# Kernel optimization log

Hardware: AMD Instinct MI355X
Metric: run time of the kernel (lower is better)

## Reference

```python
import jax, jax.numpy as jnp
import numpy as np

BETA = 2.0  # init kwarg beta


def _roi_map(roi_params, H, W):
    # roi_params: (N, K, 4) = (mu_x, mu_y, sigma_x, sigma_y) in [0, 1]
    dtype = roi_params.dtype
    gx = (jnp.arange(W, dtype=dtype) + 0.5) / W  # x-coords of grid columns
    gy = (jnp.arange(H, dtype=dtype) + 0.5) / H  # y-coords of grid rows
    mu_x, mu_y = roi_params[:, :, 0], roi_params[:, :, 1]
    sg_x, sg_y = roi_params[:, :, 2], roi_params[:, :, 3]
    # separable generalized-Gaussian log pdf along each axis
    log_x = -(jnp.abs(gx[None, None, :] - mu_x[:, :, None]) / sg_x[:, :, None]) ** BETA  # (N,K,W)
    log_y = -(jnp.abs(gy[None, None, :] - mu_y[:, :, None]) / sg_y[:, :, None]) ** BETA  # (N,K,H)
    scores = jnp.exp(log_y[:, :, :, None] + log_x[:, :, None, :])  # (N,K,H,W)
    mx = jnp.max(scores, axis=(2, 3), keepdims=True)
    return scores / (mx + 1e-12)  # max-normalized attention maps


def setup_inputs() -> dict:
    key = jax.random.key(0)
    k1, k2 = jax.random.split(key)
    x = jax.random.normal(k1, (16, 128, 128, 256), dtype=jnp.float32)
    roi_params = jax.random.uniform(k2, (16, 64, 4), dtype=jnp.float32)
    return {"x": x, "roi_params": roi_params}


def reference(x, roi_params):
    N, H, W, d = x.shape
    roi_map = _roi_map(roi_params, H, W)           # (N,K,H,W)
    flat_map = roi_map.reshape(N, -1, H * W)        # (N,K,HW)
    flat_feats = x.reshape(N, H * W, d)             # (N,HW,d)
    roi_features = jnp.einsum('nrf,nfd->nrd', flat_map, flat_feats) / (H * W)
    return roi_features, roi_params, roi_map
```

## Files before the change

### kernel.cpp

```cpp
#include <hip/hip_runtime.h>
#include <hip/hip_bf16.h>
#include <math.h>

#define NB 16
#define RB 64
#define HB 128
#define WB 128
#define DB 256
#define HW (HB * WB)

typedef __attribute__((ext_vector_type(8))) short bf16x8;
typedef __attribute__((ext_vector_type(4))) short short4v;
typedef __attribute__((ext_vector_type(4))) float f32x4;

static __device__ __forceinline__ short f2bf(float f) {
  __hip_bfloat16 h = __float2bfloat16(f);
  return *reinterpret_cast<short*>(&h);
}
static __device__ __forceinline__ float bf2f(short s) {
  return __uint_as_float(((unsigned)(unsigned short)s) << 16);
}

static __device__ __forceinline__ float axis_maxlog(float mu, float sg) {
  int i = (int)roundf(mu * 128.0f - 0.5f);
  i = i < 0 ? 0 : (i > 127 ? 127 : i);
  const float g = (i + 0.5f) * (1.0f / 128.0f);
  const float tm = fabsf(g - mu) / sg;
  return -(tm * tm);
}

__global__ __launch_bounds__(512, 4) void feat_kernel(
    const float* __restrict__ x, const float* __restrict__ roi,
    short* __restrict__ partials) {
  __shared__ float buf[2][32 * DB];

  const int bid = blockIdx.x;
  const int n   = bid >> 5;
  const int kc  = bid & 31;
  const int t   = threadIdx.x;
  const int l   = t & 63;
  const int wv  = t >> 6;
  const int mh  = wv >> 2;
  const int dw  = wv & 3;
  const int l15 = l & 15;
  const int lk  = (l >> 4) * 8;
  const int h0  = kc * 4;
  const int dbase = dw * 64 + l15 * 4;

  const f32x4* gx4 =
      reinterpret_cast<const f32x4*>(x + ((size_t)n * HW + (size_t)kc * 512) * DB);

  float mux[2], c2x[2], mlx[2];
  float eyv[4][2];
#pragma unroll
  for (int rf = 0; rf < 2; ++rf) {
    const int nr = n * RB + mh * 32 + rf * 16 + l15;
    const float4 rp = reinterpret_cast<const float4*>(roi)[nr];
    const float mlx_ = axis_maxlog(rp.x, rp.z);
    const float mly_ = axis_maxlog(rp.y, rp.w);
    const float em   = expf(mlx_ + mly_);
    const float s    = em / (em + 1e-12f);
    const float isx  = 1.0f / rp.z;
    mux[rf] = rp.x; c2x[rf] = isx * isx; mlx[rf] = mlx_;
#pragma unroll
    for (int hh = 0; hh < 4; ++hh) {
      const float g = (h0 + hh + 0.5f) * (1.0f / 128.0f);
      const float ty = fabsf(g - rp.y) / rp.w;
      eyv[hh][rf] = expf(-(ty * ty) - mly_) * s;
    }
  }

  f32x4 acc[2][4];
#pragma unroll
  for (int rf = 0; rf < 2; ++rf)
#pragma unroll
    for (int f = 0; f < 4; ++f) acc[rf][f] = (f32x4)0.0f;

  f32x4 g0, g1, g2, g3;
#define GLOAD(bi) do {                                                       \
    const f32x4* gp_ = gx4 + (size_t)(bi) * 2048;                            \
    g0 = gp_[t]; g1 = gp_[t + 512]; g2 = gp_[t + 1024]; g3 = gp_[t + 1536];  \
  } while (0)
#define DSWRITE(slot) do {                                                   \
    f32x4* lp_ = reinterpret_cast<f32x4*>(&buf[slot][0]);                    \
    lp_[t] = g0; lp_[t + 512] = g1; lp_[t + 1024] = g2; lp_[t + 1536] = g3;  \
  } while (0)

  GLOAD(0);
  DSWRITE(0);
  asm volatile("s_waitcnt lgkmcnt(0)" ::: "memory");
  __builtin_amdgcn_s_barrier();
  __builtin_amdgcn_sched_barrier(0);

#define KSTEP(bi) do {                                                       \
    if ((bi) < 15) GLOAD((bi) + 1);                                          \
    const float* bp_ = &buf[(bi) & 1][0];                                    \
    f32x4 xv_[8];                                                            \
    _Pragma("unroll")                                                        \
    for (int j = 0; j < 8; ++j)                                              \
      xv_[j] = *reinterpret_cast<const f32x4*>(                              \
          bp_ + (lk + j) * DB + dbase);                                      \
    bf16x8 bfr_[4];                                                          \
    _Pragma("unroll")                                                        \
    for (int f = 0; f < 4; ++f) {                                            \
      bf16x8 b_;                                                             \
      _Pragma("unroll")                                                      \
      for (int j = 0; j < 8; ++j) b_[j] = f2bf(xv_[j][f]);                   \
      bfr_[f] = b_;                                                          \
    }                                                                        \
    bf16x8 afr_[2];                                                          \
    _Pragma("unroll")                                                        \
    for (int rf = 0; rf < 2; ++rf) {                                         \
      const float ey_ = eyv[(bi) >> 2][rf];                                  \
      bf16x8 a_;                                                             \
      _Pragma("unroll")                                                      \
      for (int i = 0; i < 8; ++i) {                                          \
        const int col = ((bi) & 3) * 32 + lk + i;                            \
        const float g_ = (col + 0.5f) * (1.0f / 128.0f);                     \
        const float d_ = g_ - mux[rf];                                       \
        const float e_ = expf(-(d_ * d_ * c2x[rf]) - mlx[rf]);               \
        a_[i] = f2bf(ey_ * e_);                                              \
      }                                                                      \
      afr_[rf] = a_;                                                         \
    }                                                                        \
    _Pragma("unroll")                                                        \
    for (int rf = 0; rf < 2; ++rf)                                           \
      _Pragma("unroll")                                                      \
      for (int f = 0; f < 4; ++f)                                            \
        acc[rf][f] = __builtin_amdgcn_mfma_f32_16x16x32_bf16(                \
            afr_[rf], bfr_[f], acc[rf][f], 0, 0, 0);                         \
    if ((bi) < 15) DSWRITE(((bi) + 1) & 1);                                  \
    asm volatile("s_waitcnt lgkmcnt(0)" ::: "memory");                       \
    __builtin_amdgcn_s_barrier();                                            \
    __builtin_amdgcn_sched_barrier(0);                                       \
  } while (0)

  KSTEP(0);  KSTEP(1);  KSTEP(2);  KSTEP(3);
  KSTEP(4);  KSTEP(5);  KSTEP(6);  KSTEP(7);
  KSTEP(8);  KSTEP(9);  KSTEP(10); KSTEP(11);
  KSTEP(12); KSTEP(13); KSTEP(14); KSTEP(15);

#undef KSTEP
#undef DSWRITE
#undef GLOAD

  short* P = partials + (size_t)bid * (RB * DB);
#pragma unroll
  for (int rf = 0; rf < 2; ++rf) {
#pragma unroll
    for (int reg = 0; reg < 4; ++reg) {
      const int r = mh * 32 + rf * 16 + (l >> 4) * 4 + reg;
      short4v v;
      v.x = f2bf(acc[rf][0][reg]); v.y = f2bf(acc[rf][1][reg]);
      v.z = f2bf(acc[rf][2][reg]); v.w = f2bf(acc[rf][3][reg]);
      *reinterpret_cast<short4v*>(P + (size_t)r * DB + dbase) = v;
    }
  }
}

__global__ __launch_bounds__(512) void map_only_kernel(
    const float* __restrict__ roi, float* __restrict__ out_map) {
  __shared__ float sT[1024];
  const int mb = blockIdx.x;
  const int t  = threadIdx.x;
  float* sEx = sT;
  float* sEy = sT + 512;
  for (int v = t; v < 1024; v += 512) {
    const int rr = v >> 8, axis = (v >> 7) & 1, pos = v & 127;
    const float4 rp = reinterpret_cast<const float4*>(roi)[mb * 4 + rr];
    const float mlx = axis_maxlog(rp.x, rp.z);
    const float mly = axis_maxlog(rp.y, rp.w);
    const float em  = expf(mlx + mly);
    const float s   = em / (em + 1e-12f);
    const float g   = (pos + 0.5f) * (1.0f / 128.0f);
    if (axis == 0) {
      const float tx = fabsf(g - rp.x) / rp.z;
      sEx[rr * 128 + pos] = expf(-(tx * tx) - mlx);
    } else {
      const float ty = fabsf(g - rp.y) / rp.w;
      sEy[rr * 128 + pos] = expf(-(ty * ty) - mly) * s;
    }
  }
  __syncthreads();
  f32x4* dst = reinterpret_cast<f32x4*>(out_map + (size_t)mb * 4 * HW);
#pragma unroll
  for (int p = 0; p < 32; ++p) {
    const int idx = p * 512 + t;
    const int rr = idx >> 12, h = (idx >> 5) & 127, w4 = idx & 31;
    const f32x4 e = *reinterpret_cast<const f32x4*>(&sEx[rr * 128 + w4 * 4]);
    dst[idx] = e * (f32x4)sEy[rr * 128 + h];
  }
}

__global__ __launch_bounds__(256) void reduce_kernel(
    const short* __restrict__ partials, const float* __restrict__ roi,
    float* __restrict__ outF, float* __restrict__ out_params) {
  const int idx = blockIdx.x * 256 + threadIdx.x;
  const int n   = idx >> 12;
  const int i4  = idx & 4095;
  const short4v* p =
      reinterpret_cast<const short4v*>(partials) + (size_t)n * 32 * 4096 + i4;
  f32x4 s = (f32x4)0.0f;
#pragma unroll
  for (int kc = 0; kc < 32; ++kc) {
    const short4v v = p[(size_t)kc * 4096];
    s.x += bf2f(v.x); s.y += bf2f(v.y); s.z += bf2f(v.z); s.w += bf2f(v.w);
  }
  s *= (1.0f / (float)HW);
  reinterpret_cast<f32x4*>(outF)[idx] = s;
  if (idx < NB * RB * 4) out_params[idx] = roi[idx];
}

extern "C" void kernel_launch(void* const* d_in, const int* in_sizes, int n_in,
                              void* d_out, int out_size, void* d_ws, size_t ws_size,
                              hipStream_t stream) {
  const float* x   = (const float*)d_in[0];
  const float* roi = (const float*)d_in[1];
  float* out        = (float*)d_out;
  float* out_feat   = out;
  float* out_params = out + NB * RB * DB;
  float* out_map    = out_params + NB * RB * 4;

  const size_t par_shorts = 512u * RB * DB;
  const bool ws_ok = ws_size >= par_shorts * sizeof(short) + 64;

  short* P = ws_ok ? (short*)d_ws : (short*)out_map;

  feat_kernel<<<512, 512, 0, stream>>>(x, roi, P);
  reduce_kernel<<<256, 256, 0, stream>>>(P, roi, out_feat, out_params);
  map_only_kernel<<<256, 512, 0, stream>>>(roi, out_map);
}
```

Before: 99.62 us.

## Fuse map writer into feat kernel, drop LDS staging, widen per-wave ROI tile

```diff
diff --git a/kernel.cpp b/kernel.cpp
--- a/kernel.cpp
+++ b/kernel.cpp
@@ -8,6 +8,7 @@
 #define WB 128
 #define DB 256
 #define HW (HB * WB)
+#define LOG2E 1.4426950408889634f
 
 typedef __attribute__((ext_vector_type(8))) short bf16x8;
 typedef __attribute__((ext_vector_type(4))) short short4v;
@@ -29,39 +30,72 @@
   return -(tm * tm);
 }
 
-__global__ __launch_bounds__(512, 4) void feat_kernel(
+template <bool WITHMAP>
+__global__ __launch_bounds__(256, 2) void feat_kernel(
     const float* __restrict__ x, const float* __restrict__ roi,
-    short* __restrict__ partials) {
-  __shared__ float buf[2][32 * DB];
+    short* __restrict__ partials, float* __restrict__ out_map) {
+  __shared__ float sT[1024];
 
   const int bid = blockIdx.x;
+  const int t   = threadIdx.x;
+
+  if (WITHMAP && bid >= 512) {
+    const int mb = bid - 512;
+    float* sEx = sT;
+    float* sEy = sT + 512;
+    for (int v = t; v < 1024; v += 256) {
+      const int rr = v >> 8, axis = (v >> 7) & 1, pos = v & 127;
+      const float4 rp = reinterpret_cast<const float4*>(roi)[mb * 4 + rr];
+      const float mlx = axis_maxlog(rp.x, rp.z);
+      const float mly = axis_maxlog(rp.y, rp.w);
+      const float em  = expf(mlx + mly);
+      const float s   = em / (em + 1e-12f);
+      const float g   = (pos + 0.5f) * (1.0f / 128.0f);
+      if (axis == 0) {
+        const float tx = fabsf(g - rp.x) / rp.z;
+        sEx[rr * 128 + pos] = expf(-(tx * tx) - mlx);
+      } else {
+        const float ty = fabsf(g - rp.y) / rp.w;
+        sEy[rr * 128 + pos] = expf(-(ty * ty) - mly) * s;
+      }
+    }
+    __syncthreads();
+    f32x4* dst = reinterpret_cast<f32x4*>(out_map + (size_t)mb * 4 * HW);
+#pragma unroll 8
+    for (int p = 0; p < 64; ++p) {
+      const int idx = p * 256 + t;
+      const int rr = idx >> 12, h = (idx >> 5) & 127, w4 = idx & 31;
+      const f32x4 e = *reinterpret_cast<const f32x4*>(&sEx[rr * 128 + w4 * 4]);
+      dst[idx] = e * (f32x4)sEy[rr * 128 + h];
+    }
+    return;
+  }
+
   const int n   = bid >> 5;
-  const int kc  = bid & 31;
-  const int t   = threadIdx.x;
+  const int hc  = bid & 31;
   const int l   = t & 63;
   const int wv  = t >> 6;
-  const int mh  = wv >> 2;
-  const int dw  = wv & 3;
   const int l15 = l & 15;
   const int lk  = (l >> 4) * 8;
-  const int h0  = kc * 4;
-  const int dbase = dw * 64 + l15 * 4;
+  const int h0  = hc * 4;
+  const int dbase = wv * 64 + l15 * 4;
 
   const f32x4* gx4 =
-      reinterpret_cast<const f32x4*>(x + ((size_t)n * HW + (size_t)kc * 512) * DB);
-
-  float mux[2], c2x[2], mlx[2];
-  float eyv[4][2];
-#pragma unroll
-  for (int rf = 0; rf < 2; ++rf) {
-    const int nr = n * RB + mh * 32 + rf * 16 + l15;
+      reinterpret_cast<const f32x4*>(x + ((size_t)n * HW + (size_t)hc * 512) * DB);
+  const int lquad = wv * 16 + l15;
+
+  float mux[4], c2x[4], mlx2[4];
+  float eyv[4][4];
+#pragma unroll
+  for (int rf = 0; rf < 4; ++rf) {
+    const int nr = n * RB + rf * 16 + l15;
     const float4 rp = reinterpret_cast<const float4*>(roi)[nr];
     const float mlx_ = axis_maxlog(rp.x, rp.z);
     const float mly_ = axis_maxlog(rp.y, rp.w);
     const float em   = expf(mlx_ + mly_);
     const float s    = em / (em + 1e-12f);
     const float isx  = 1.0f / rp.z;
-    mux[rf] = rp.x; c2x[rf] = isx * isx; mlx[rf] = mlx_;
+    mux[rf] = rp.x; c2x[rf] = isx * isx * LOG2E; mlx2[rf] = mlx_ * LOG2E;
 #pragma unroll
     for (int hh = 0; hh < 4; ++hh) {
       const float g = (h0 + hh + 0.5f) * (1.0f / 128.0f);
@@ -70,47 +104,33 @@
     }
   }
 
-  f32x4 acc[2][4];
-#pragma unroll
-  for (int rf = 0; rf < 2; ++rf)
+  f32x4 acc[4][4];
+#pragma unroll
+  for (int rf = 0; rf < 4; ++rf)
 #pragma unroll
     for (int f = 0; f < 4; ++f) acc[rf][f] = (f32x4)0.0f;
 
-  f32x4 g0, g1, g2, g3;
-#define GLOAD(bi) do {                                                       \
-    const f32x4* gp_ = gx4 + (size_t)(bi) * 2048;                            \
-    g0 = gp_[t]; g1 = gp_[t + 512]; g2 = gp_[t + 1024]; g3 = gp_[t + 1536];  \
+  f32x4 xva[8], xvb[8];
+
+#define GLOAD(BUFN, bi) do {                                                 \
+    _Pragma("unroll")                                                        \
+    for (int j = 0; j < 8; ++j)                                              \
+      BUFN[j] = gx4[(size_t)((bi) * 32 + lk + j) * 64 + lquad];              \
   } while (0)
-#define DSWRITE(slot) do {                                                   \
-    f32x4* lp_ = reinterpret_cast<f32x4*>(&buf[slot][0]);                    \
-    lp_[t] = g0; lp_[t + 512] = g1; lp_[t + 1024] = g2; lp_[t + 1536] = g3;  \
-  } while (0)
-
-  GLOAD(0);
-  DSWRITE(0);
-  asm volatile("s_waitcnt lgkmcnt(0)" ::: "memory");
-  __builtin_amdgcn_s_barrier();
-  __builtin_amdgcn_sched_barrier(0);
-
-#define KSTEP(bi) do {                                                       \
-    if ((bi) < 15) GLOAD((bi) + 1);                                          \
-    const float* bp_ = &buf[(bi) & 1][0];                                    \
-    f32x4 xv_[8];                                                            \
-    _Pragma("unroll")                                                        \
-    for (int j = 0; j < 8; ++j)                                              \
-      xv_[j] = *reinterpret_cast<const f32x4*>(                              \
-          bp_ + (lk + j) * DB + dbase);                                      \
+
+#define KSTEP(bi, CUR, NXT) do {                                             \
+    if ((bi) < 15) GLOAD(NXT, (bi) + 1);                                     \
     bf16x8 bfr_[4];                                                          \
     _Pragma("unroll")                                                        \
     for (int f = 0; f < 4; ++f) {                                            \
       bf16x8 b_;                                                             \
       _Pragma("unroll")                                                      \
-      for (int j = 0; j < 8; ++j) b_[j] = f2bf(xv_[j][f]);                   \
+      for (int j = 0; j < 8; ++j) b_[j] = f2bf(CUR[j][f]);                   \
       bfr_[f] = b_;                                                          \
     }                                                                        \
-    bf16x8 afr_[2];                                                          \
-    _Pragma("unroll")                                                        \
-    for (int rf = 0; rf < 2; ++rf) {                                         \
+    bf16x8 afr_[4];                                                          \
+    _Pragma("unroll")                                                        \
+    for (int rf = 0; rf < 4; ++rf) {                                         \
       const float ey_ = eyv[(bi) >> 2][rf];                                  \
       bf16x8 a_;                                                             \
       _Pragma("unroll")                                                      \
@@ -118,38 +138,36 @@
         const int col = ((bi) & 3) * 32 + lk + i;                            \
         const float g_ = (col + 0.5f) * (1.0f / 128.0f);                     \
         const float d_ = g_ - mux[rf];                                       \
-        const float e_ = expf(-(d_ * d_ * c2x[rf]) - mlx[rf]);               \
+        const float e_ = exp2f(-(d_ * d_ * c2x[rf]) - mlx2[rf]);             \
         a_[i] = f2bf(ey_ * e_);                                              \
       }                                                                      \
       afr_[rf] = a_;                                                         \
     }                                                                        \
     _Pragma("unroll")                                                        \
-    for (int rf = 0; rf < 2; ++rf)                                           \
+    for (int rf = 0; rf < 4; ++rf)                                           \
       _Pragma("unroll")                                                      \
       for (int f = 0; f < 4; ++f)                                            \
         acc[rf][f] = __builtin_amdgcn_mfma_f32_16x16x32_bf16(                \
             afr_[rf], bfr_[f], acc[rf][f], 0, 0, 0);                         \
-    if ((bi) < 15) DSWRITE(((bi) + 1) & 1);                                  \
-    asm volatile("s_waitcnt lgkmcnt(0)" ::: "memory");                       \
-    __builtin_amdgcn_s_barrier();                                            \
-    __builtin_amdgcn_sched_barrier(0);                                       \
   } while (0)
 
-  KSTEP(0);  KSTEP(1);  KSTEP(2);  KSTEP(3);
-  KSTEP(4);  KSTEP(5);  KSTEP(6);  KSTEP(7);
-  KSTEP(8);  KSTEP(9);  KSTEP(10); KSTEP(11);
-  KSTEP(12); KSTEP(13); KSTEP(14); KSTEP(15);
+  GLOAD(xva, 0);
+  KSTEP(0,  xva, xvb); KSTEP(1,  xvb, xva); KSTEP(2,  xva, xvb);
+  KSTEP(3,  xvb, xva); KSTEP(4,  xva, xvb); KSTEP(5,  xvb, xva);
+  KSTEP(6,  xva, xvb); KSTEP(7,  xvb, xva); KSTEP(8,  xva, xvb);
+  KSTEP(9,  xvb, xva); KSTEP(10, xva, xvb); KSTEP(11, xvb, xva);
+  KSTEP(12, xva, xvb); KSTEP(13, xvb, xva); KSTEP(14, xva, xvb);
+  KSTEP(15, xvb, xva);
 
 #undef KSTEP
-#undef DSWRITE
 #undef GLOAD
 
   short* P = partials + (size_t)bid * (RB * DB);
 #pragma unroll
-  for (int rf = 0; rf < 2; ++rf) {
+  for (int rf = 0; rf < 4; ++rf) {
 #pragma unroll
     for (int reg = 0; reg < 4; ++reg) {
-      const int r = mh * 32 + rf * 16 + (l >> 4) * 4 + reg;
+      const int r = rf * 16 + (l >> 4) * 4 + reg;
       short4v v;
       v.x = f2bf(acc[rf][0][reg]); v.y = f2bf(acc[rf][1][reg]);
       v.z = f2bf(acc[rf][2][reg]); v.w = f2bf(acc[rf][3][reg]);
@@ -158,14 +176,14 @@
   }
 }
 
-__global__ __launch_bounds__(512) void map_only_kernel(
+__global__ __launch_bounds__(256) void map_only_kernel(
     const float* __restrict__ roi, float* __restrict__ out_map) {
   __shared__ float sT[1024];
   const int mb = blockIdx.x;
   const int t  = threadIdx.x;
   float* sEx = sT;
   float* sEy = sT + 512;
-  for (int v = t; v < 1024; v += 512) {
+  for (int v = t; v < 1024; v += 256) {
     const int rr = v >> 8, axis = (v >> 7) & 1, pos = v & 127;
     const float4 rp = reinterpret_cast<const float4*>(roi)[mb * 4 + rr];
     const float mlx = axis_maxlog(rp.x, rp.z);
@@ -183,9 +201,9 @@
   }
   __syncthreads();
   f32x4* dst = reinterpret_cast<f32x4*>(out_map + (size_t)mb * 4 * HW);
-#pragma unroll
-  for (int p = 0; p < 32; ++p) {
-    const int idx = p * 512 + t;
+#pragma unroll 8
+  for (int p = 0; p < 64; ++p) {
+    const int idx = p * 256 + t;
     const int rr = idx >> 12, h = (idx >> 5) & 127, w4 = idx & 31;
     const f32x4 e = *reinterpret_cast<const f32x4*>(&sEx[rr * 128 + w4 * 4]);
     dst[idx] = e * (f32x4)sEy[rr * 128 + h];
@@ -224,9 +242,14 @@
   const size_t par_shorts = 512u * RB * DB;
   const bool ws_ok = ws_size >= par_shorts * sizeof(short) + 64;
 
-  short* P = ws_ok ? (short*)d_ws : (short*)out_map;
-
-  feat_kernel<<<512, 512, 0, stream>>>(x, roi, P);
-  reduce_kernel<<<256, 256, 0, stream>>>(P, roi, out_feat, out_params);
-  map_only_kernel<<<256, 512, 0, stream>>>(roi, out_map);
-}
+  if (ws_ok) {
+    short* P = (short*)d_ws;
+    feat_kernel<true><<<768, 256, 0, stream>>>(x, roi, P, out_map);
+    reduce_kernel<<<256, 256, 0, stream>>>(P, roi, out_feat, out_params);
+  } else {
+    short* P = (short*)out_map;
+    feat_kernel<false><<<512, 256, 0, stream>>>(x, roi, P, out_map);
+    reduce_kernel<<<256, 256, 0, stream>>>(P, roi, out_feat, out_params);
+    map_only_kernel<<<256, 256, 0, stream>>>(roi, out_map);
+  }
+}
```

Result: no change. 99.12 us (-0.5%).
